# Performance work log

Hardware: AMD Instinct MI355X
Metric: run time of the kernel (lower is better)

## Reference

```python
import jax, jax.numpy as jnp
import numpy as np
from jax import lax

DN = ('NCHW', 'OIHW', 'NCHW')
BN_EPS = 1e-5
LRELU_SLOPE = 0.01


def conv_block(x, w1, b1, w2, b2, gamma, bn_bias):
    # Conv2d(512->256, k=1) -> Conv2d(256->512, k=3, pad=1) -> LeakyReLU -> BatchNorm2d(512)
    y = lax.conv_general_dilated(x, w1, (1, 1), 'VALID', dimension_numbers=DN)
    y = y + b1[None, :, None, None]
    y = lax.conv_general_dilated(y, w2, (1, 1), 'SAME', dimension_numbers=DN)
    y = y + b2[None, :, None, None]
    y = jnp.where(y > 0, y, LRELU_SLOPE * y)
    # BatchNorm2d in training mode: batch statistics over (B, H, W) per channel
    mean = jnp.mean(y, axis=(0, 2, 3))
    var = jnp.var(y, axis=(0, 2, 3))
    y = (y - mean[None, :, None, None]) * lax.rsqrt(var + BN_EPS)[None, :, None, None]
    return y * gamma[None, :, None, None] + bn_bias[None, :, None, None]


def setup_inputs() -> dict:
    key = jax.random.key(0)
    ks = jax.random.split(key, 9)
    B, C, H, W = 8, 512, 32, 32
    x = jax.random.normal(ks[0], (B, C, H, W), dtype=jnp.float32)
    x1 = jax.random.normal(ks[1], (B, C, H, W), dtype=jnp.float32)
    x2 = jax.random.normal(ks[2], (B, C, H, W), dtype=jnp.float32)
    w1 = jax.random.normal(ks[3], (256, 512, 1, 1), dtype=jnp.float32) * 0.02
    b1 = jnp.zeros((256,), dtype=jnp.float32)
    w2 = jax.random.normal(ks[4], (512, 256, 3, 3), dtype=jnp.float32) * 0.02
    b2 = jnp.zeros((512,), dtype=jnp.float32)
    gamma = jnp.ones((512,), dtype=jnp.float32)
    bn_bias = jnp.zeros((512,), dtype=jnp.float32)
    beta = jax.random.normal(ks[5], (1,), dtype=jnp.float32)  # Parameter(zeros(1)) in torch; random so output is non-trivial
    return {"x": x, "x1": x1, "x2": x2, "w1": w1, "b1": b1, "w2": w2,
            "b2": b2, "gamma": gamma, "bn_bias": bn_bias, "beta": beta}


def reference(x, x1, x2, w1, b1, w2, b2, gamma, bn_bias, beta):
    B, C, H, W = x1.shape
    N = H * W
    F1 = conv_block(x1, w1, b1, w2, b2, gamma, bn_bias).reshape(B, C, N)   # [B, C, N]
    F2 = conv_block(x2, w1, b1, w2, b2, gamma, bn_bias).reshape(B, C, N)   # [B, C, N]
    scores = jnp.einsum('bcn,bdn->bcd', F1, F2)                            # [B, C, C]
    attention = jax.nn.softmax(scores, axis=-1)
    out = jnp.einsum('bcd,bdn->bcn', attention, x.reshape(B, C, N))
    return beta * out.reshape(B, C, H, W)
```

## Files before the change

### kernel.cpp

```cpp
#include <hip/hip_runtime.h>


typedef __attribute__((ext_vector_type(8))) short bfrag;
typedef __attribute__((ext_vector_type(4))) float facc;

__device__ __forceinline__ unsigned short bf16_rn(float v) {
  unsigned u = __float_as_uint(v);
  return (unsigned short)((u + 0x7fffu + ((u >> 16) & 1u)) >> 16);
}

__device__ __forceinline__ void dma16(const void* g, const void* lds) {
  __builtin_amdgcn_global_load_lds(
      (const __attribute__((address_space(1))) unsigned int*)g,
      (__attribute__((address_space(3))) unsigned int*)(unsigned int)(unsigned long long)(const char*)lds,
      16, 0, 0);
}

__global__ __launch_bounds__(256) void prologue(
    const float* __restrict__ x1, const float* __restrict__ x2,
    const float* __restrict__ w2, unsigned char* __restrict__ x12timg,
    unsigned short* __restrict__ w2s, float* __restrict__ statsz) {
  int bid = blockIdx.x;
  int t = threadIdx.x;
  if (bid < 8192) {
    __shared__ float tile[32][33];
    int p0 = (bid & 31) * 32, ci0 = ((bid >> 5) & 15) * 32, z = bid >> 9;
    const float* src = (z < 8) ? x1 + (size_t)z * 524288 : x2 + (size_t)(z - 8) * 524288;
    {
      int ci_l = t >> 5, p_l = t & 31;
#pragma unroll
      for (int j = 0; j < 4; j++)
        tile[ci_l + 8 * j][p_l] = src[(size_t)(ci0 + ci_l + 8 * j) * 1024 + p0 + p_l];
    }
    __syncthreads();
    {
      int p_l = t >> 3, cg = (t & 7) * 4;
      unsigned short hh[4], ll[4];
#pragma unroll
      for (int j = 0; j < 4; j++) {
        float v = tile[cg + j][p_l];
        hh[j] = bf16_rn(v);
        ll[j] = bf16_rn(v - __uint_as_float((unsigned)hh[j] << 16));
      }
      int px = p0 + p_l, row = px & 127, panel = px >> 7;
      int c = ci0 + cg, kc = c >> 6, ck = (c >> 3) & 7;
      int slot = ck ^ (row & 7);
      size_t byte = (((size_t)(z * 8 + panel) * 8 + kc) * 128 + row) * 256 + slot * 16 + (c & 7) * 2;
      *(ushort4*)(x12timg + byte) = make_ushort4(hh[0], hh[1], hh[2], hh[3]);
      *(ushort4*)(x12timg + byte + 128) = make_ushort4(ll[0], ll[1], ll[2], ll[3]);
    }
  } else {
    int co = bid - 8192;
    if (co < 40) statsz[co * 256 + t] = 0.f;
    int panel = co >> 7, coh = (co >> 6) & 1, jf = (co >> 4) & 3, lmv = co & 15;
    int chunk = t >> 5, qv = (t >> 3) & 3, e = t & 7;
    int lanev = qv * 16 + lmv;
    const float* src = w2 + ((size_t)co * 256 + t) * 9;
#pragma unroll
    for (int tap = 0; tap < 9; tap++) {
      float v = src[tap];
      unsigned short h = bf16_rn(v);
      unsigned short l = bf16_rn(v - __uint_as_float((unsigned)h << 16));
      int P = (panel * 8 + chunk) * 9 + tap;
      size_t us = (((size_t)(P * 2 + coh) * 8 + jf * 2) * 512) + lanev * 8 + e;
      w2s[us] = h;
      w2s[us + 512] = l;
    }
  }
}

__global__ __launch_bounds__(256) void transpose_split_x(
    const float* __restrict__ x, unsigned char* __restrict__ img) {
  __shared__ float tile[32][33];
  int z = blockIdx.z;
  const float* src = x + (size_t)z * 524288;
  int ci0 = blockIdx.y * 32, p0 = blockIdx.x * 32;
  int t = threadIdx.x;
  {
    int ci_l = t >> 5, p_l = t & 31;
#pragma unroll
    for (int j = 0; j < 4; j++)
      tile[ci_l + 8 * j][p_l] = src[(size_t)(ci0 + ci_l + 8 * j) * 1024 + p0 + p_l];
  }
  __syncthreads();
  {
    int p_l = t >> 3, cg = (t & 7) * 4;
    unsigned short hh[4], ll[4];
#pragma unroll
    for (int j = 0; j < 4; j++) {
      float v = tile[cg + j][p_l];
      hh[j] = bf16_rn(v);
      ll[j] = bf16_rn(v - __uint_as_float((unsigned)hh[j] << 16));
    }
    int px = p0 + p_l, row = px & 127, panel = px >> 7;
    int c = ci0 + cg, kc = c >> 6, ck = (c >> 3) & 7;
    int slot = ck ^ (row & 7);
    size_t byte = (((size_t)(z * 8 + panel) * 8 + kc) * 128 + row) * 256 + slot * 16 + (c & 7) * 2;
    *(ushort4*)(img + byte) = make_ushort4(hh[0], hh[1], hh[2], hh[3]);
    *(ushort4*)(img + byte + 128) = make_ushort4(ll[0], ll[1], ll[2], ll[3]);
  }
}

template <int KTOT, int EPI, int AF32, int KSPLIT>
__global__ __launch_bounds__(256, 2) void gemm_nt(
    const void* __restrict__ Asrc, long long aZS, int aKC,
    const unsigned char* __restrict__ Bimg, long long bZS, int bKC,
    void* __restrict__ out0,
    const float* __restrict__ p0, const float* __restrict__ p1,
    const float* __restrict__ p2, const float* __restrict__ p3) {
  __shared__ __attribute__((aligned(16))) unsigned char smem[49152];
  int t = threadIdx.x;
  int z = blockIdx.z;
  int zb = z, kh = 0;
  if (KSPLIT) { zb = z & 7; kh = z >> 3; }
  int m0 = blockIdx.y * 128, n0 = blockIdx.x * 64;
  int w = t >> 6, lane = t & 63;
  int lm = lane & 15, q = lane >> 4;
  int mh = (w & 1) * 64, nh = (w >> 1) * 32;
  const unsigned char* Abase = (const unsigned char*)Asrc + (size_t)zb * aZS +
      (size_t)(m0 >> 7) * ((size_t)aKC << 15) + (size_t)w * 8192 + (size_t)lane * 16;
  const unsigned char* Bbase = Bimg + (size_t)zb * bZS +
      (size_t)(n0 >> 7) * ((size_t)bKC << 15) + (size_t)(n0 & 127) * 256 +
      (size_t)w * 4096 + (size_t)lane * 16;
  facc acc[4][2] = {};
  for (int k0 = 0; k0 < KTOT; k0 += 64) {
    int kc = (KSPLIT ? kh * (KTOT / 64) : 0) + (k0 >> 6);
    __syncthreads();
    if (AF32) {
      const float* Af = (const float*)Asrc;
#pragma unroll
      for (int j = 0; j < 8; j++) {
        int idx = t + 256 * j;
        int row = idx >> 4, c4 = idx & 15;
        float4 v = *(const float4*)(Af + (size_t)(m0 + row) * KTOT + k0 + c4 * 4);
        unsigned short h0 = bf16_rn(v.x), h1 = bf16_rn(v.y), h2 = bf16_rn(v.z), h3 = bf16_rn(v.w);
        unsigned short l0 = bf16_rn(v.x - __uint_as_float((unsigned)h0 << 16));
        unsigned short l1 = bf16_rn(v.y - __uint_as_float((unsigned)h1 << 16));
        unsigned short l2 = bf16_rn(v.z - __uint_as_float((unsigned)h2 << 16));
        unsigned short l3 = bf16_rn(v.w - __uint_as_float((unsigned)h3 << 16));
        int base = row * 256 + (((c4 >> 1) ^ (row & 7)) * 16) + (c4 & 1) * 8;
        *(ushort4*)(smem + base) = make_ushort4(h0, h1, h2, h3);
        *(ushort4*)(smem + base + 128) = make_ushort4(l0, l1, l2, l3);
      }
    } else {
      const unsigned char* ap = Abase + ((size_t)kc << 15);
#pragma unroll
      for (int j = 0; j < 8; j++) dma16(ap + j * 1024, smem + w * 8192 + j * 1024);
    }
    {
      const unsigned char* bp = Bbase + ((size_t)kc << 15);
#pragma unroll
      for (int j = 0; j < 4; j++) dma16(bp + j * 1024, smem + 32768 + w * 4096 + j * 1024);
    }
    __syncthreads();
#pragma unroll
    for (int ks = 0; ks < 2; ks++) {
      bfrag ah[4], al[4], bh[2], bl[2];
#pragma unroll
      for (int mt = 0; mt < 4; mt++) {
        int m = mh + mt * 16 + lm;
        int phys = ((ks * 4 + q) ^ (m & 7)) * 16;
        const unsigned char* p = smem + m * 256 + phys;
        ah[mt] = *(const bfrag*)p;
        al[mt] = *(const bfrag*)(p + 128);
      }
#pragma unroll
      for (int nt = 0; nt < 2; nt++) {
        int n = nh + nt * 16 + lm;
        int phys = ((ks * 4 + q) ^ (n & 7)) * 16;
        const unsigned char* p = smem + 32768 + n * 256 + phys;
        bh[nt] = *(const bfrag*)p;
        bl[nt] = *(const bfrag*)(p + 128);
      }
#pragma unroll
      for (int mt = 0; mt < 4; mt++)
#pragma unroll
        for (int nt = 0; nt < 2; nt++) {
          acc[mt][nt] = __builtin_amdgcn_mfma_f32_16x16x32_bf16(ah[mt], bh[nt], acc[mt][nt], 0, 0, 0);
          acc[mt][nt] = __builtin_amdgcn_mfma_f32_16x16x32_bf16(ah[mt], bl[nt], acc[mt][nt], 0, 0, 0);
          acc[mt][nt] = __builtin_amdgcn_mfma_f32_16x16x32_bf16(al[mt], bh[nt], acc[mt][nt], 0, 0, 0);
        }
    }
  }
  if (EPI == 0) {
    unsigned char* Yimg = (unsigned char*)out0;
    int g = zb;
#pragma unroll
    for (int mt = 0; mt < 4; mt++) {
      int mb = m0 + mh + mt * 16 + q * 4;
      int ch = mb >> 5, chunk = (mb >> 3) & 3, e2 = (mb & 7) * 2;
#pragma unroll
      for (int nt = 0; nt < 2; nt++) {
        int px = n0 + nh + nt * 16 + lm;
        int gy = px >> 5, gx = px & 31;
        int slot = chunk ^ ((gx + 1) & 7);
        size_t base = ((size_t)((g * 8 + ch) * 32 + gy)) * 4096 + gx * 128 + slot * 16 + e2;
        unsigned short hh[4], ll[4];
#pragma unroll
        for (int r = 0; r < 4; r++) {
          float v = acc[mt][nt][r] + p0[mb + r];
          hh[r] = bf16_rn(v);
          ll[r] = bf16_rn(v - __uint_as_float((unsigned)hh[r] << 16));
        }
        *(ushort4*)(Yimg + base) = make_ushort4(hh[0], hh[1], hh[2], hh[3]);
        *(ushort4*)(Yimg + (base ^ 64)) = make_ushort4(ll[0], ll[1], ll[2], ll[3]);
      }
    }
  } else if (EPI == 1) {
    float* S = (float*)out0 + (size_t)kh * 2097152;
    const float* stats = p0;
    const float* rowsum = p1;
    const float* gamma = p2;
    const float* bnb = p3;
    float a2v[2], t2v[2], r2v[2];
#pragma unroll
    for (int nt = 0; nt < 2; nt++) {
      int d = n0 + nh + nt * 16 + lm;
      float mu = stats[512 + d] * (1.f / 8192.f);
      float var = stats[1536 + d] * (1.f / 8192.f) - mu * mu;
      float a = gamma[d] * rsqrtf(var + 1e-5f);
      a2v[nt] = a;
      t2v[nt] = bnb[d] - mu * a;
      r2v[nt] = rowsum[(8 + zb) * 512 + d];
    }
#pragma unroll
    for (int mt = 0; mt < 4; mt++)
#pragma unroll
      for (int r = 0; r < 4; r++) {
        int cc = m0 + mh + mt * 16 + q * 4 + r;
        float mu = stats[cc] * (1.f / 8192.f);
        float var = stats[1024 + cc] * (1.f / 8192.f) - mu * mu;
        float a1 = gamma[cc] * rsqrtf(var + 1e-5f);
        float t1 = bnb[cc] - mu * a1;
        float r1 = rowsum[zb * 512 + cc];
#pragma unroll
        for (int nt = 0; nt < 2; nt++) {
          int d = n0 + nh + nt * 16 + lm;
          float sc = a1 * a2v[nt] * acc[mt][nt][r];
          if (kh == 0)
            sc += a1 * t2v[nt] * r1 + t1 * a2v[nt] * r2v[nt] + 1024.f * t1 * t2v[nt];
          S[((size_t)(zb * 512 + cc)) * 512 + d] = sc;
        }
      }
  } else {
    float* O = (float*)out0;
    float sc = p0[0];
#pragma unroll
    for (int mt = 0; mt < 4; mt++)
#pragma unroll
      for (int r = 0; r < 4; r++) {
        int cc = m0 + mh + mt * 16 + q * 4 + r;
#pragma unroll
        for (int nt = 0; nt < 2; nt++) {
          int n = n0 + nh + nt * 16 + lm;
          O[((size_t)(zb * 512 + cc)) * 1024 + n] = sc * acc[mt][nt][r];
        }
      }
  }
}

__global__ __launch_bounds__(256, 2) void conv3x3_mfma(
    const unsigned char* __restrict__ Yimg, const unsigned short* __restrict__ w2s,
    const float* __restrict__ b2, unsigned char* __restrict__ Fimg,
    float* __restrict__ stats, float* __restrict__ rowsum) {
  __shared__ __attribute__((aligned(16))) unsigned char smem[2][26112];
  int t = threadIdx.x;
  int g = blockIdx.z;
  int panel = blockIdx.y;
  int co_base = panel * 128;
  int y0 = blockIdx.x * 4;
  int w = t >> 6, lane = t & 63;
  int lm = lane & 15, q = lane >> 4;
  int co_half = (w & 1) * 64, px_half = (w >> 1) * 64;
  int px_l[4], row_l[4], x_l[4];
#pragma unroll
  for (int i = 0; i < 4; i++) {
    px_l[i] = px_half + i * 16 + lm;
    row_l[i] = px_l[i] >> 5;
    x_l[i] = px_l[i] & 31;
  }
  auto stageIn = [&](int ct, unsigned char* dst) {
#pragma unroll
    for (int jj = 0; jj < 6; jj++) {
      int id = w * 6 + jj;
      int strip = id >> 2, part = id & 3;
      int gy = y0 - 1 + strip;
      if ((unsigned)gy < 32u) {
        const unsigned char* srcp = Yimg +
            ((size_t)((g * 8 + ct) * 32 + gy)) * 4096 + part * 1024 + lane * 16;
        dma16(srcp, dst + strip * 4352 + 128 + part * 1024);
      }
    }
  };
  for (int u = t; u < 3264; u += 256)
    *(uint4*)(&smem[0][0] + (size_t)u * 16) = make_uint4(0u, 0u, 0u, 0u);
  __syncthreads();
  stageIn(0, &smem[0][0]);
  __syncthreads();
  const unsigned char* wg0 = (const unsigned char*)w2s +
      (size_t)panel * 72 * 16384 + (size_t)(w & 1) * 8192 + (size_t)lane * 16;
  facc acc[4][4] = {};
#pragma unroll 1
  for (int c = 0; c < 8; c++) {
    const unsigned char* bufp = &smem[c & 1][0];
    const unsigned char* wpc = wg0 + (((size_t)c * 9) << 14);
#pragma unroll
    for (int r = 0; r < 9; r++) {
      const int dy = r / 3, dx = r % 3;
      bfrag W[8];
#pragma unroll
      for (int u = 0; u < 8; u++)
        W[u] = *(const bfrag*)(wpc + (((size_t)r) << 14) + u * 1024);
      if (r == 3 && c < 7) stageIn(c + 1, &smem[(c + 1) & 1][0]);
      bfrag bh[4], bl[4];
#pragma unroll
      for (int i = 0; i < 4; i++) {
        int xh = x_l[i] + dx;
        int entry = (row_l[i] + dy) * 34 + xh;
        const unsigned char* pb = bufp + entry * 128;
        int ph = (q ^ (xh & 7)) * 16;
        bh[i] = *(const bfrag*)(pb + ph);
        bl[i] = *(const bfrag*)(pb + (ph ^ 64));
      }
#pragma unroll
      for (int j = 0; j < 4; j++)
#pragma unroll
        for (int i = 0; i < 4; i++) {
          acc[j][i] = __builtin_amdgcn_mfma_f32_16x16x32_bf16(W[2 * j], bh[i], acc[j][i], 0, 0, 0);
          acc[j][i] = __builtin_amdgcn_mfma_f32_16x16x32_bf16(W[2 * j], bl[i], acc[j][i], 0, 0, 0);
          acc[j][i] = __builtin_amdgcn_mfma_f32_16x16x32_bf16(W[2 * j + 1], bh[i], acc[j][i], 0, 0, 0);
        }
    }
    __syncthreads();
  }
  int grp = g >> 3;
  int px0 = blockIdx.x * 128;
#pragma unroll
  for (int j = 0; j < 4; j++) {
#pragma unroll
    for (int r = 0; r < 4; r++) {
      int co = co_base + co_half + j * 16 + q * 4 + r;
      int row = co & 127;
      float bb = b2[co];
      float s = 0.f, s2 = 0.f;
#pragma unroll
      for (int i = 0; i < 4; i++) {
        float v = acc[j][i][r] + bb;
        v = v > 0.f ? v : 0.01f * v;
        unsigned short h = bf16_rn(v);
        unsigned short l = bf16_rn(v - __uint_as_float((unsigned)h << 16));
        int px = px0 + px_l[i];
        int kc = px >> 6, ck = (px >> 3) & 7;
        int slot = ck ^ (row & 7);
        size_t byte = (((size_t)(g * 4 + panel) * 16 + kc) * 128 + row) * 256 +
                      slot * 16 + (px & 7) * 2;
        *(unsigned short*)(Fimg + byte) = h;
        *(unsigned short*)(Fimg + byte + 128) = l;
        s += v;
        s2 = fmaf(v, v, s2);
      }
#pragma unroll
      for (int d = 1; d <= 8; d <<= 1) {
        s += __shfl_xor(s, d);
        s2 += __shfl_xor(s2, d);
      }
      if (lm == 0) {
        atomicAdd(&stats[grp * 512 + co], s);
        atomicAdd(&stats[1024 + grp * 512 + co], s2);
        atomicAdd(&rowsum[g * 512 + co], s);
      }
    }
  }
}

__global__ __launch_bounds__(256) void softmax_rows(const float* __restrict__ S,
                                                    unsigned char* __restrict__ attimg) {
  int rowg = blockIdx.x;
  int z = rowg >> 9, c = rowg & 511;
  const float* p = S + (size_t)rowg * 512;
  const float* p1 = p + 2097152;
  int t = threadIdx.x;
  float2 va = *(const float2*)(p + 2 * t);
  float2 vb = *(const float2*)(p1 + 2 * t);
  float vx = va.x + vb.x, vy = va.y + vb.y;
  float mx = fmaxf(vx, vy);
#pragma unroll
  for (int d = 32; d >= 1; d >>= 1) mx = fmaxf(mx, __shfl_xor(mx, d));
  __shared__ float sred[8];
  int wave = t >> 6, lane = t & 63;
  if (lane == 0) sred[wave] = mx;
  __syncthreads();
  float m4 = fmaxf(fmaxf(sred[0], sred[1]), fmaxf(sred[2], sred[3]));
  float ex = expf(vx - m4), ey = expf(vy - m4);
  float s = ex + ey;
#pragma unroll
  for (int d = 32; d >= 1; d >>= 1) s += __shfl_xor(s, d);
  if (lane == 0) sred[4 + wave] = s;
  __syncthreads();
  float inv = 1.f / (sred[4] + sred[5] + sred[6] + sred[7]);
  float px_ = ex * inv, py_ = ey * inv;
  unsigned short h0 = bf16_rn(px_), h1 = bf16_rn(py_);
  unsigned short l0 = bf16_rn(px_ - __uint_as_float((unsigned)h0 << 16));
  unsigned short l1 = bf16_rn(py_ - __uint_as_float((unsigned)h1 << 16));
  int rowl = c & 127, panel = c >> 7;
  int d0 = 2 * t;
  int kc = d0 >> 6, ck = (d0 >> 3) & 7;
  int slot = ck ^ (rowl & 7);
  size_t byte = (((size_t)(z * 4 + panel) * 8 + kc) * 128 + rowl) * 256 +
                slot * 16 + (d0 & 7) * 2;
  *(ushort2*)(attimg + byte) = make_ushort2(h0, h1);
  *(ushort2*)(attimg + byte + 128) = make_ushort2(l0, l1);
}

extern "C" void kernel_launch(void* const* d_in, const int* in_sizes, int n_in,
                              void* d_out, int out_size, void* d_ws, size_t ws_size,
                              hipStream_t stream) {
  const float* x = (const float*)d_in[0];
  const float* x1 = (const float*)d_in[1];
  const float* x2 = (const float*)d_in[2];
  const float* w1 = (const float*)d_in[3];
  const float* b1 = (const float*)d_in[4];
  const float* w2 = (const float*)d_in[5];
  const float* b2 = (const float*)d_in[6];
  const float* gamma = (const float*)d_in[7];
  const float* bnb = (const float*)d_in[8];
  const float* beta = (const float*)d_in[9];
  float* out = (float*)d_out;
  unsigned char* wsb = (unsigned char*)d_ws;

  unsigned char* x12timg = wsb;
  unsigned char* Fimg = wsb;
  unsigned char* xtimg = wsb;
  unsigned char* attimg = wsb + 16777216;
  unsigned char* Yimg = wsb + 33554432;
  float* S = (float*)(wsb + 33554432);
  unsigned short* w2s = (unsigned short*)(wsb + 50331648);
  float* stats = (float*)(wsb + 55050240);
  float* rowsum = (float*)(wsb + 55058432);

  prologue<<<8704, 256, 0, stream>>>(x1, x2, w2, x12timg, w2s, stats);
  gemm_nt<512, 0, 1, 0><<<dim3(16, 2, 16), 256, 0, stream>>>(
      w1, 0LL, 0, x12timg, 2097152LL, 8, Yimg, b1, nullptr, nullptr, nullptr);
  conv3x3_mfma<<<dim3(8, 4, 16), 256, 0, stream>>>(
      Yimg, w2s, b2, Fimg, stats, rowsum);
  gemm_nt<512, 1, 0, 1><<<dim3(8, 4, 16), 256, 0, stream>>>(
      Fimg, 2097152LL, 16, Fimg + (size_t)8 * 2097152, 2097152LL, 16,
      S, stats, rowsum, gamma, bnb);
  transpose_split_x<<<dim3(32, 16, 8), 256, 0, stream>>>(x, xtimg);
  softmax_rows<<<4096, 256, 0, stream>>>(S, attimg);
  gemm_nt<512, 2, 0, 0><<<dim3(16, 4, 8), 256, 0, stream>>>(
      attimg, 1048576LL, 8, xtimg, 2097152LL, 8, out, beta, nullptr, nullptr, nullptr);
}
```

Measured before the change: 299.0 us.

## Stage conv3x3 weights through LDS and pipeline input rows in a ring buffer

Weights for the 3x3 conv are now repacked into an XOR-swizzled row layout and double-buffered into LDS per tap via global_load_lds, instead of each wave loading weight fragments directly from global memory. Input rows are kept in an 8-slot ring of row strips that is refilled incrementally across taps, rather than double-buffering full channel tiles. This is meant to hide global weight-load latency and cut redundant global traffic. In exchange it adds a __syncthreads per tap instead of per channel chunk and raises LDS use to about 66 KB, which may lower occupancy.

```diff
diff --git a/kernel.cpp b/kernel.cpp
--- a/kernel.cpp
+++ b/kernel.cpp
@@ -52,9 +52,9 @@
   } else {
     int co = bid - 8192;
     if (co < 40) statsz[co * 256 + t] = 0.f;
-    int panel = co >> 7, coh = (co >> 6) & 1, jf = (co >> 4) & 3, lmv = co & 15;
-    int chunk = t >> 5, qv = (t >> 3) & 3, e = t & 7;
-    int lanev = qv * 16 + lmv;
+    int panel = co >> 7, co_l = co & 127;
+    int chunk = t >> 5, q = (t >> 3) & 3, e = t & 7;
+    int slot = q ^ (co_l & 7);
     const float* src = w2 + ((size_t)co * 256 + t) * 9;
 #pragma unroll
     for (int tap = 0; tap < 9; tap++) {
@@ -62,9 +62,9 @@
       unsigned short h = bf16_rn(v);
       unsigned short l = bf16_rn(v - __uint_as_float((unsigned)h << 16));
       int P = (panel * 8 + chunk) * 9 + tap;
-      size_t us = (((size_t)(P * 2 + coh) * 8 + jf * 2) * 512) + lanev * 8 + e;
+      size_t us = (size_t)P * 8192 + co_l * 64 + slot * 8 + e;
       w2s[us] = h;
-      w2s[us + 512] = l;
+      w2s[us ^ 32] = l;
     }
   }
 }
@@ -263,7 +263,8 @@
     const unsigned char* __restrict__ Yimg, const unsigned short* __restrict__ w2s,
     const float* __restrict__ b2, unsigned char* __restrict__ Fimg,
     float* __restrict__ stats, float* __restrict__ rowsum) {
-  __shared__ __attribute__((aligned(16))) unsigned char smem[2][26112];
+  __shared__ __attribute__((aligned(16))) unsigned char smem[67584];
+  const int WOFF = 34816;
   int t = threadIdx.x;
   int g = blockIdx.z;
   int panel = blockIdx.y;
@@ -272,6 +273,7 @@
   int w = t >> 6, lane = t & 63;
   int lm = lane & 15, q = lane >> 4;
   int co_half = (w & 1) * 64, px_half = (w >> 1) * 64;
+  int pha = (q ^ (lm & 7)) * 16;
   int px_l[4], row_l[4], x_l[4];
 #pragma unroll
   for (int i = 0; i < 4; i++) {
@@ -279,45 +281,67 @@
     row_l[i] = px_l[i] >> 5;
     x_l[i] = px_l[i] & 31;
   }
-  auto stageIn = [&](int ct, unsigned char* dst) {
-#pragma unroll
-    for (int jj = 0; jj < 6; jj++) {
-      int id = w * 6 + jj;
-      int strip = id >> 2, part = id & 3;
-      int gy = y0 - 1 + strip;
-      if ((unsigned)gy < 32u) {
-        const unsigned char* srcp = Yimg +
-            ((size_t)((g * 8 + ct) * 32 + gy)) * 4096 + part * 1024 + lane * 16;
-        dma16(srcp, dst + strip * 4352 + 128 + part * 1024);
-      }
-    }
+  const unsigned char* w2sb = (const unsigned char*)w2s + (((size_t)panel * 72) << 14);
+  auto stageW = [&](int P) {
+    const unsigned char* srcp = w2sb + (((size_t)P) << 14) + (w * 4) * 1024 + lane * 16;
+    unsigned char* dstp = smem + WOFF + ((P & 1) << 14) + (w * 4) * 1024;
+#pragma unroll
+    for (int j = 0; j < 4; j++) dma16(srcp + j * 1024, dstp + j * 1024);
   };
-  for (int u = t; u < 3264; u += 256)
-    *(uint4*)(&smem[0][0] + (size_t)u * 16) = make_uint4(0u, 0u, 0u, 0u);
+  auto stageStrip = [&](int slot, int gy, int cc) {
+    unsigned char* dst = smem + slot * 4352 + 128 + w * 1024;
+    if ((unsigned)gy < 32u) {
+      const unsigned char* srcp = Yimg +
+          ((size_t)((g * 8 + cc) * 32 + gy)) * 4096 + w * 1024 + lane * 16;
+      dma16(srcp, dst);
+    } else {
+      *(uint4*)(dst + lane * 16) = make_uint4(0u, 0u, 0u, 0u);
+    }
+  };
+  for (int u = t; u < 2176; u += 256)
+    *(uint4*)(smem + (size_t)u * 16) = make_uint4(0u, 0u, 0u, 0u);
   __syncthreads();
-  stageIn(0, &smem[0][0]);
+  stageW(0);
+  stageStrip(0, y0 - 1, 0);
+  stageStrip(1, y0 + 0, 0);
+  stageStrip(2, y0 + 1, 0);
+  stageStrip(3, y0 + 2, 0);
   __syncthreads();
-  const unsigned char* wg0 = (const unsigned char*)w2s +
-      (size_t)panel * 72 * 16384 + (size_t)(w & 1) * 8192 + (size_t)lane * 16;
   facc acc[4][4] = {};
 #pragma unroll 1
   for (int c = 0; c < 8; c++) {
-    const unsigned char* bufp = &smem[c & 1][0];
-    const unsigned char* wpc = wg0 + (((size_t)c * 9) << 14);
-#pragma unroll
-    for (int r = 0; r < 9; r++) {
-      const int dy = r / 3, dx = r % 3;
-      bfrag W[8];
-#pragma unroll
-      for (int u = 0; u < 8; u++)
-        W[u] = *(const bfrag*)(wpc + (((size_t)r) << 14) + u * 1024);
-      if (r == 3 && c < 7) stageIn(c + 1, &smem[(c + 1) & 1][0]);
-      bfrag bh[4], bl[4];
+    int base6 = (c * 6) & 7;
+#pragma unroll
+    for (int tap = 0; tap < 9; tap++) {
+      const int dy = tap / 3, dx = tap % 3;
+      int p = c * 9 + tap;
+      if (p < 71) stageW(p + 1);
+      if (tap == 0) {
+        stageStrip((base6 + 4) & 7, y0 + 3, c);
+        stageStrip((base6 + 5) & 7, y0 + 4, c);
+        if (c < 7) {
+          stageStrip((base6 + 6) & 7, y0 - 1, c + 1);
+          stageStrip((base6 + 7) & 7, y0 + 0, c + 1);
+        }
+      } else if (tap == 3) {
+        if (c < 7) stageStrip(base6, y0 + 1, c + 1);
+      } else if (tap == 6) {
+        if (c < 7) stageStrip((base6 + 1) & 7, y0 + 2, c + 1);
+      }
+      const unsigned char* wb = smem + WOFF + ((p & 1) << 14);
+      bfrag ah[4], al[4], bh[4], bl[4];
+#pragma unroll
+      for (int j = 0; j < 4; j++) {
+        int co_r = co_half + j * 16 + lm;
+        const unsigned char* pa = wb + co_r * 128;
+        ah[j] = *(const bfrag*)(pa + pha);
+        al[j] = *(const bfrag*)(pa + (pha ^ 64));
+      }
 #pragma unroll
       for (int i = 0; i < 4; i++) {
         int xh = x_l[i] + dx;
-        int entry = (row_l[i] + dy) * 34 + xh;
-        const unsigned char* pb = bufp + entry * 128;
+        int slot = (base6 + row_l[i] + dy) & 7;
+        const unsigned char* pb = smem + slot * 4352 + xh * 128;
         int ph = (q ^ (xh & 7)) * 16;
         bh[i] = *(const bfrag*)(pb + ph);
         bl[i] = *(const bfrag*)(pb + (ph ^ 64));
@@ -326,12 +350,12 @@
       for (int j = 0; j < 4; j++)
 #pragma unroll
         for (int i = 0; i < 4; i++) {
-          acc[j][i] = __builtin_amdgcn_mfma_f32_16x16x32_bf16(W[2 * j], bh[i], acc[j][i], 0, 0, 0);
-          acc[j][i] = __builtin_amdgcn_mfma_f32_16x16x32_bf16(W[2 * j], bl[i], acc[j][i], 0, 0, 0);
-          acc[j][i] = __builtin_amdgcn_mfma_f32_16x16x32_bf16(W[2 * j + 1], bh[i], acc[j][i], 0, 0, 0);
-        }
-    }
-    __syncthreads();
+          acc[j][i] = __builtin_amdgcn_mfma_f32_16x16x32_bf16(ah[j], bh[i], acc[j][i], 0, 0, 0);
+          acc[j][i] = __builtin_amdgcn_mfma_f32_16x16x32_bf16(ah[j], bl[i], acc[j][i], 0, 0, 0);
+          acc[j][i] = __builtin_amdgcn_mfma_f32_16x16x32_bf16(al[j], bh[i], acc[j][i], 0, 0, 0);
+        }
+      __syncthreads();
+    }
   }
   int grp = g >> 3;
   int px0 = blockIdx.x * 128;
```

Result: faster. 291.3 us (-2.6%).
